# Kernel tuning notes

Measured on AMD Instinct MI355X. Metric: run time of the kernel, lower is better.

The kernel has to match this reference:

```python
import jax, jax.numpy as jnp
import numpy as np

HIDDEN = 512
SEQ = 2048
BATCH = 64


def setup_inputs() -> dict:
    key = jax.random.key(0)
    k1, k2 = jax.random.split(key)
    x = jax.random.normal(k1, (SEQ, BATCH, HIDDEN), dtype=jnp.float32)
    # weight_hh ~ uniform(0, 1) as in reset_parameters
    weight_hh = jax.random.uniform(k2, (HIDDEN,), dtype=jnp.float32)
    return {"x": x, "weight_hh": weight_hh}


def reference(x, weight_hh):
    # IndRNN (recurrent-only): h_t = relu(x_t + w_hh * h_{t-1})
    # x: [T, B, H], weight_hh: [H]
    h0 = jnp.zeros((x.shape[1], x.shape[2]), dtype=x.dtype)

    def step(h, x_t):
        h_new = jax.nn.relu(x_t + h * weight_hh)  # [B, H]
        return h_new, h_new

    _, outputs = jax.lax.scan(step, h0, x)  # outputs: [T, B, H]
    return outputs
```

## Files before the change

### kernel.cpp

```cpp
#include <hip/hip_runtime.h>


#define HIDDEN 512
#define SEQ 2048
#define BATCH 64

constexpr int STRIDE = BATCH * HIDDEN;
constexpr int CHAINS = BATCH * HIDDEN;
constexpr int WAVES = 8;
constexpr int BLOCK = WAVES * 64;
constexpr int LWIN = SEQ / WAVES;
constexpr int DEPTH = 16;

template <bool PF>
__device__ __forceinline__ void rec_chunk(float& hv, const float wh,
                                          const float (&cur)[DEPTH],
                                          float (&nxt)[DEPTH],
                                          const float* __restrict__ xn,
                                          float* __restrict__ o) {
#pragma unroll
  for (int i = 0; i < DEPTH; ++i) {
    if (PF) nxt[i] = __builtin_nontemporal_load(xn + (long)i * STRIDE);
    hv = fmaxf(0.0f, fmaf(wh, hv, cur[i]));
    __builtin_nontemporal_store(hv, o + (long)i * STRIDE);
  }
}

template <bool PF>
__device__ __forceinline__ void comp_chunk(float& C, float& Bv, float& Sv,
                                           const float wh,
                                           const float (&cur)[DEPTH],
                                           float (&nxt)[DEPTH],
                                           const float* __restrict__ xn) {
#pragma unroll
  for (int i = 0; i < DEPTH; ++i) {
    if (PF) nxt[i] = cur ? 0.0f : 0.0f;
  }
}

template <bool PF>
__device__ __forceinline__ void comp_chunk2(float& C, float& Bv, float& Sv,
                                            const float wh,
                                            const float (&cur)[DEPTH],
                                            float (&nxt)[DEPTH],
                                            const float* __restrict__ xn) {
#pragma unroll
  for (int i = 0; i < DEPTH; ++i) {
    if (PF) nxt[i] = xn[(long)i * STRIDE];
    const float xv = cur[i];
    C = fmaxf(0.0f, fmaf(wh, C, xv));
    Bv = fmaf(wh, Bv, xv);
    Sv *= wh;
  }
}

__global__ __launch_bounds__(BLOCK) void indrnn_scan(
    const float* __restrict__ x, const float* __restrict__ w,
    float* __restrict__ out) {
  __shared__ float sC[WAVES][64];
  __shared__ float sB[WAVES][64];
  __shared__ float sS[WAVES][64];

  const int lane = threadIdx.x & 63;
  const int wv = threadIdx.x >> 6;
  const int chain = blockIdx.x * 64 + lane;
  const float wh = w[chain & (HIDDEN - 1)];

  const long base = (long)(wv * LWIN) * STRIDE + chain;
  const float* xp = x + base;
  float* op = out + base;

  float bufA[DEPTH], bufB[DEPTH];
#pragma unroll
  for (int i = 0; i < DEPTH; ++i) bufA[i] = xp[(long)i * STRIDE];

  if (wv == 0) {
    float hv = 0.0f;
    int t = 0;
#pragma unroll 1
    for (; t + 2 * DEPTH < LWIN; t += 2 * DEPTH) {
      rec_chunk<true>(hv, wh, bufA, bufB, xp + (long)(t + DEPTH) * STRIDE,
                      op + (long)t * STRIDE);
      rec_chunk<true>(hv, wh, bufB, bufA, xp + (long)(t + 2 * DEPTH) * STRIDE,
                      op + (long)(t + DEPTH) * STRIDE);
    }
    rec_chunk<true>(hv, wh, bufA, bufB, xp + (long)(t + DEPTH) * STRIDE,
                    op + (long)t * STRIDE);
    rec_chunk<false>(hv, wh, bufB, bufA, nullptr,
                     op + (long)(t + DEPTH) * STRIDE);
    sC[0][lane] = hv;
  } else {
    float C = 0.0f, Bv = 0.0f, Sv = 1.0f;
    int t = 0;
#pragma unroll 1
    for (; t + 2 * DEPTH < LWIN; t += 2 * DEPTH) {
      comp_chunk2<true>(C, Bv, Sv, wh, bufA, bufB,
                        xp + (long)(t + DEPTH) * STRIDE);
      comp_chunk2<true>(C, Bv, Sv, wh, bufB, bufA,
                        xp + (long)(t + 2 * DEPTH) * STRIDE);
    }
    comp_chunk2<true>(C, Bv, Sv, wh, bufA, bufB,
                      xp + (long)(t + DEPTH) * STRIDE);
    comp_chunk2<false>(C, Bv, Sv, wh, bufB, bufA, nullptr);

#pragma unroll
    for (int i = 0; i < DEPTH; ++i)
      bufA[i] = __builtin_nontemporal_load(xp + (long)i * STRIDE);

    sC[wv][lane] = C;
    sB[wv][lane] = Bv;
    sS[wv][lane] = Sv;
  }

  __syncthreads();

  if (wv == 0) return;

  float hv = sC[0][lane];
  for (int k = 1; k < wv; ++k)
    hv = fmaxf(sC[k][lane], fmaf(sS[k][lane], hv, sB[k][lane]));

  int t = 0;
#pragma unroll 1
  for (; t + 2 * DEPTH < LWIN; t += 2 * DEPTH) {
    rec_chunk<true>(hv, wh, bufA, bufB, xp + (long)(t + DEPTH) * STRIDE,
                    op + (long)t * STRIDE);
    rec_chunk<true>(hv, wh, bufB, bufA, xp + (long)(t + 2 * DEPTH) * STRIDE,
                    op + (long)(t + DEPTH) * STRIDE);
  }
  rec_chunk<true>(hv, wh, bufA, bufB, xp + (long)(t + DEPTH) * STRIDE,
                  op + (long)t * STRIDE);
  rec_chunk<false>(hv, wh, bufB, bufA, nullptr,
                   op + (long)(t + DEPTH) * STRIDE);
}

extern "C" void kernel_launch(void* const* d_in, const int* in_sizes, int n_in,
                              void* d_out, int out_size, void* d_ws,
                              size_t ws_size, hipStream_t stream) {
  const float* x = (const float*)d_in[0];
  const float* w = (const float*)d_in[1];
  float* out = (float*)d_out;
  indrnn_scan<<<CHAINS / 64, BLOCK, 0, stream>>>(x, w, out);
}
```

Baseline: 478.8 us.

## Double scan waves per block, halve prefetch depth, compute window decay analytically

Splits each chain's time axis across 16 waves instead of 8, so each wave handles a shorter window and the serial phases get shorter. Prefetch depth drops to 8 to relieve register pressure, and launch bounds are tightened. The per-window decay product w^LWIN is no longer carried through the scan and stored in shared memory; it is computed by repeated squaring (w^128). That squaring count is hardcoded to LWIN=128 and only holds for these constants. The combine loop grows with more waves, and the larger blocks may lower occupancy.

```diff
diff --git a/kernel.cpp b/kernel.cpp
--- a/kernel.cpp
+++ b/kernel.cpp
@@ -7,10 +7,10 @@
 
 constexpr int STRIDE = BATCH * HIDDEN;
 constexpr int CHAINS = BATCH * HIDDEN;
-constexpr int WAVES = 8;
+constexpr int WAVES = 16;
 constexpr int BLOCK = WAVES * 64;
 constexpr int LWIN = SEQ / WAVES;
-constexpr int DEPTH = 16;
+constexpr int DEPTH = 8;
 
 template <bool PF>
 __device__ __forceinline__ void rec_chunk(float& hv, const float wh,
@@ -27,39 +27,24 @@
 }
 
 template <bool PF>
-__device__ __forceinline__ void comp_chunk(float& C, float& Bv, float& Sv,
-                                           const float wh,
+__device__ __forceinline__ void comp_chunk(float& C, float& Bv, const float wh,
                                            const float (&cur)[DEPTH],
                                            float (&nxt)[DEPTH],
                                            const float* __restrict__ xn) {
-#pragma unroll
-  for (int i = 0; i < DEPTH; ++i) {
-    if (PF) nxt[i] = cur ? 0.0f : 0.0f;
-  }
-}
-
-template <bool PF>
-__device__ __forceinline__ void comp_chunk2(float& C, float& Bv, float& Sv,
-                                            const float wh,
-                                            const float (&cur)[DEPTH],
-                                            float (&nxt)[DEPTH],
-                                            const float* __restrict__ xn) {
 #pragma unroll
   for (int i = 0; i < DEPTH; ++i) {
     if (PF) nxt[i] = xn[(long)i * STRIDE];
     const float xv = cur[i];
     C = fmaxf(0.0f, fmaf(wh, C, xv));
     Bv = fmaf(wh, Bv, xv);
-    Sv *= wh;
   }
 }
 
-__global__ __launch_bounds__(BLOCK) void indrnn_scan(
+__global__ __launch_bounds__(BLOCK, 8) void indrnn_scan(
     const float* __restrict__ x, const float* __restrict__ w,
     float* __restrict__ out) {
   __shared__ float sC[WAVES][64];
   __shared__ float sB[WAVES][64];
-  __shared__ float sS[WAVES][64];
 
   const int lane = threadIdx.x & 63;
   const int wv = threadIdx.x >> 6;
@@ -90,18 +75,17 @@
                      op + (long)(t + DEPTH) * STRIDE);
     sC[0][lane] = hv;
   } else {
-    float C = 0.0f, Bv = 0.0f, Sv = 1.0f;
+    float C = 0.0f, Bv = 0.0f;
     int t = 0;
 #pragma unroll 1
     for (; t + 2 * DEPTH < LWIN; t += 2 * DEPTH) {
-      comp_chunk2<true>(C, Bv, Sv, wh, bufA, bufB,
-                        xp + (long)(t + DEPTH) * STRIDE);
-      comp_chunk2<true>(C, Bv, Sv, wh, bufB, bufA,
-                        xp + (long)(t + 2 * DEPTH) * STRIDE);
+      comp_chunk<true>(C, Bv, wh, bufA, bufB,
+                       xp + (long)(t + DEPTH) * STRIDE);
+      comp_chunk<true>(C, Bv, wh, bufB, bufA,
+                       xp + (long)(t + 2 * DEPTH) * STRIDE);
     }
-    comp_chunk2<true>(C, Bv, Sv, wh, bufA, bufB,
-                      xp + (long)(t + DEPTH) * STRIDE);
-    comp_chunk2<false>(C, Bv, Sv, wh, bufB, bufA, nullptr);
+    comp_chunk<true>(C, Bv, wh, bufA, bufB, xp + (long)(t + DEPTH) * STRIDE);
+    comp_chunk<false>(C, Bv, wh, bufB, bufA, nullptr);
 
 #pragma unroll
     for (int i = 0; i < DEPTH; ++i)
@@ -109,16 +93,19 @@
 
     sC[wv][lane] = C;
     sB[wv][lane] = Bv;
-    sS[wv][lane] = Sv;
   }
 
   __syncthreads();
 
   if (wv == 0) return;
 
+  float Spow = wh;
+#pragma unroll
+  for (int k = 0; k < 7; ++k) Spow *= Spow;
+
   float hv = sC[0][lane];
   for (int k = 1; k < wv; ++k)
-    hv = fmaxf(sC[k][lane], fmaf(sS[k][lane], hv, sB[k][lane]));
+    hv = fmaxf(sC[k][lane], fmaf(Spow, hv, sB[k][lane]));
 
   int t = 0;
 #pragma unroll 1
```

Result: no change. 487.0 us (+1.7%).
